# Kernel tuning notes

Hardware: AMD Instinct MI355X
Metric: run time of the kernel (lower is better)

The kernel has to match this reference:

```python
import jax, jax.numpy as jnp
import numpy as np
from jax import lax

NUM_GROUP = 512
GROUP_SIZE = 32


def fps(xyz, npoint):
    """Farthest point sampling. xyz: [B, N, 3] -> centers [B, npoint, 3]."""
    B, N, _ = xyz.shape
    big = jnp.asarray(1e10, xyz.dtype)

    def body(carry, _):
        min_d, farthest = carry  # [B, N], [B]
        centroid = jnp.take_along_axis(xyz, farthest[:, None, None], axis=1)  # [B,1,3]
        d = jnp.sum((xyz - centroid) ** 2, axis=-1)  # [B, N]
        min_d = jnp.minimum(min_d, d)
        nxt = jnp.argmax(min_d, axis=-1).astype(jnp.int32)
        return (min_d, nxt), farthest

    init = (jnp.full((B, N), big, xyz.dtype), jnp.zeros((B,), jnp.int32))
    _, idxs = lax.scan(body, init, None, length=npoint)  # [npoint, B]
    idxs = idxs.T  # [B, npoint]
    return jnp.take_along_axis(xyz, idxs[..., None], axis=1)  # [B, npoint, 3]


def knn_idx(xyz, center, k):
    """xyz [B,N,3], center [B,G,3] -> idx [B,G,k] of k nearest (squared L2)."""
    # [B, G, N] squared distances
    d2 = jnp.sum((center[:, :, None, :] - xyz[:, None, :, :]) ** 2, axis=-1)
    _, idx = lax.top_k(-d2, k)  # smallest distances
    return idx


def setup_inputs() -> dict:
    key = jax.random.key(0)
    xyz = jax.random.normal(key, (32, 3, 8192), dtype=jnp.float32)
    return {"xyz": xyz}


def reference(xyz):
    # xyz: [B, 3, N] -> [B, N, 3]
    pts = jnp.transpose(xyz, (0, 2, 1))[:, :, :3]
    B, N, _ = pts.shape
    center = fps(pts, NUM_GROUP)                  # [B, G, 3]
    idx = knn_idx(pts, center, GROUP_SIZE)        # [B, G, k]
    flat_idx = idx.reshape(B, NUM_GROUP * GROUP_SIZE)
    neighborhood = jnp.take_along_axis(pts, flat_idx[..., None], axis=1)
    neighborhood = neighborhood.reshape(B, NUM_GROUP, GROUP_SIZE, 3)
    neighborhood = neighborhood - center[:, :, None, :]
    return neighborhood, center
```

## Files before the change

kernel.cpp:

```cpp
#include <hip/hip_runtime.h>

typedef unsigned long long u64;
typedef unsigned int u32;
typedef float v2f __attribute__((ext_vector_type(2)));

#define BATCH 32
#define NPTS  8192
#define NGRP  512
#define KNN_K 32

#define FPS_T 256
#define FPS_W (FPS_T / 64)
#define PPAIR (NPTS / FPS_T / 2)
#define KNN_WPB 4
#define QCAP 128

__device__ __forceinline__ float sq3(float dx, float dy, float dz) {
    return __fadd_rn(__fadd_rn(__fmul_rn(dx, dx), __fmul_rn(dy, dy)), __fmul_rn(dz, dz));
}

__device__ __forceinline__ u64 packdi(float d, int n) {
    return ((u64)__float_as_uint(d) << 32) | (u32)n;
}

__device__ __forceinline__ u64 umin64(u64 a, u64 b) { return a < b ? a : b; }
__device__ __forceinline__ u64 umax64(u64 a, u64 b) { return a > b ? a : b; }

__device__ __forceinline__ u64 shfl_xor_u64(u64 v, int m) {
    int lo = __shfl_xor((int)(u32)v, m, 64);
    int hi = __shfl_xor((int)(u32)(v >> 32), m, 64);
    return ((u64)(u32)hi << 32) | (u32)lo;
}

__device__ __forceinline__ u64 shfl_u64(u64 v, int src) {
    int lo = __shfl((int)(u32)v, src, 64);
    int hi = __shfl((int)(u32)(v >> 32), src, 64);
    return ((u64)(u32)hi << 32) | (u32)lo;
}

template <int CTRL>
__device__ __forceinline__ u64 dpp_max_step(u64 k) {
    u32 plo = (u32)__builtin_amdgcn_update_dpp(0, (int)(u32)k, CTRL, 0xF, 0xF, true);
    u32 phi = (u32)__builtin_amdgcn_update_dpp(0, (int)(u32)(k >> 32), CTRL, 0xF, 0xF, true);
    u64 p = ((u64)phi << 32) | plo;
    return k > p ? k : p;
}
__device__ __forceinline__ u64 dpp_wave_max(u64 k) {
    k = dpp_max_step<0x111>(k);
    k = dpp_max_step<0x112>(k);
    k = dpp_max_step<0x114>(k);
    k = dpp_max_step<0x118>(k);
    k = dpp_max_step<0x142>(k);
    k = dpp_max_step<0x143>(k);
    return k;
}

__device__ __forceinline__ u64 lane_sort64(u64 v, int lane) {
#pragma unroll
    for (int k = 2; k <= 64; k <<= 1) {
#pragma unroll
        for (int j = k >> 1; j > 0; j >>= 1) {
            u64 p = shfl_xor_u64(v, j);
            bool keepmin = (((lane & k) == 0) == ((lane & j) == 0));
            u64 mn = umin64(v, p), mx = umax64(v, p);
            v = keepmin ? mn : mx;
        }
    }
    return v;
}

__device__ __forceinline__ u64 lane_merge64(u64 m, u64 c, int lane) {
    u64 cr = shfl_xor_u64(c, 63);
    u64 z = umin64(m, cr);
#pragma unroll
    for (int dd = 32; dd > 0; dd >>= 1) {
        u64 p = shfl_xor_u64(z, dd);
        u64 mn = umin64(z, p), mx = umax64(z, p);
        z = (lane & dd) ? mx : mn;
    }
    return z;
}

__global__ __launch_bounds__(FPS_T) void fps_kernel(const float* __restrict__ in,
                                                    float* __restrict__ centers) {
#pragma clang fp contract(off)
    __shared__ float sx[NPTS];
    __shared__ float sy[NPTS];
    __shared__ float sz[NPTS];
    __shared__ u64 s_key[2][FPS_W];
    __shared__ float s_out[NGRP * 3];

    const int b = blockIdx.x;
    const int t = threadIdx.x;
    const int w = t >> 6;
    const float* xp = in + (size_t)b * 3 * NPTS;
    const float* yp = xp + NPTS;
    const float* zp = xp + 2 * NPTS;

    v2f xr[PPAIR], yr[PPAIR], zr[PPAIR], md[PPAIR];
#pragma unroll
    for (int i = 0; i < PPAIR; ++i) {
        int n = i * (2 * FPS_T) + 2 * t;
        xr[i] = *(const v2f*)(xp + n);
        yr[i] = *(const v2f*)(yp + n);
        zr[i] = *(const v2f*)(zp + n);
        *(v2f*)(sx + n) = xr[i];
        *(v2f*)(sy + n) = yr[i];
        *(v2f*)(sz + n) = zr[i];
        md[i] = (v2f){1e10f, 1e10f};
    }
    __syncthreads();

    int cur = 0;
    for (int r = 0; r < NGRP; ++r) {
        const float cx = sx[cur], cy = sy[cur], cz = sz[cur];
        if (t == 0) {
            s_out[r * 3 + 0] = cx;
            s_out[r * 3 + 1] = cy;
            s_out[r * 3 + 2] = cz;
        }

        float bd0 = -1.0f, bd1 = -1.0f;
        int   bi0 = 0,     bi1 = 0;
#pragma unroll
        for (int i = 0; i < PPAIR; ++i) {
            v2f dx = xr[i] - cx;
            v2f dy = yr[i] - cy;
            v2f dz = zr[i] - cz;
            v2f dd = dx * dx + dy * dy + dz * dz;
            md[i] = __builtin_elementwise_min(md[i], dd);
            int n = i * (2 * FPS_T) + 2 * t;
            if (md[i].x > bd0) { bd0 = md[i].x; bi0 = n; }
            if (md[i].y > bd1) { bd1 = md[i].y; bi1 = n + 1; }
        }
        u64 k0 = ((u64)__float_as_uint(bd0) << 32) | (u32)(~(u32)bi0);
        u64 k1 = ((u64)__float_as_uint(bd1) << 32) | (u32)(~(u32)bi1);
        u64 k = dpp_wave_max(umax64(k0, k1));
        if ((t & 63) == 63) s_key[r & 1][w] = k;
        __syncthreads();
        u64 m = umax64(umax64(s_key[r & 1][0], s_key[r & 1][1]),
                       umax64(s_key[r & 1][2], s_key[r & 1][3]));
        cur = (int)(~(u32)m);
    }

    __syncthreads();
    float* cdst = centers + (size_t)b * NGRP * 3;
    for (int i = t; i < NGRP * 3; i += FPS_T) cdst[i] = s_out[i];
}

__global__ __launch_bounds__(KNN_WPB * 64) void knn_kernel(const float* __restrict__ in,
                                                           const float* __restrict__ centers,
                                                           float* __restrict__ out) {
    __shared__ u64 sbuf[KNN_WPB][QCAP];

    const int wave = threadIdx.x >> 6;
    const int lane = threadIdx.x & 63;
    const int cid  = blockIdx.x * KNN_WPB + wave;
    const int b    = cid >> 9;

    const float* xp = in + (size_t)b * 3 * NPTS;
    const float* yp = xp + NPTS;
    const float* zp = xp + 2 * NPTS;

    const float cx = centers[cid * 3 + 0];
    const float cy = centers[cid * 3 + 1];
    const float cz = centers[cid * 3 + 2];

    float x = xp[lane], y = yp[lane], z = zp[lane];
    u64 m = packdi(sq3(__fsub_rn(x, cx), __fsub_rn(y, cy), __fsub_rn(z, cz)), lane);
    m = lane_sort64(m, lane);
    u64 tau = shfl_u64(m, 31);
    int cnt = 0;

    float nx = xp[64 + lane], ny = yp[64 + lane], nz = zp[64 + lane];
#pragma unroll 1
    for (int j = 1; j < NPTS / 64; ++j) {
        x = nx; y = ny; z = nz;
        if (j + 1 < NPTS / 64) {
            int n2 = (j + 1) * 64 + lane;
            nx = xp[n2]; ny = yp[n2]; nz = zp[n2];
        }
        float d = sq3(__fsub_rn(x, cx), __fsub_rn(y, cy), __fsub_rn(z, cz));
        u64 kk = packdi(d, j * 64 + lane);
        bool cand = kk < tau;
        u64 mask = __ballot(cand);
        if (mask) {
            u32 below = __builtin_amdgcn_mbcnt_hi(
                (u32)(mask >> 32), __builtin_amdgcn_mbcnt_lo((u32)mask, 0));
            if (cand) sbuf[wave][cnt + below] = kk;
            cnt += (int)__popcll(mask);
            if (cnt >= 64) {
                u64 c = sbuf[wave][lane];
                c = lane_sort64(c, lane);
                m = lane_merge64(m, c, lane);
                tau = shfl_u64(m, 31);
                int rem = cnt - 64;
                if (lane < rem) sbuf[wave][lane] = sbuf[wave][64 + lane];
                cnt = rem;
            }
        }
    }
    while (cnt > 0) {
        int take = cnt < 64 ? cnt : 64;
        u64 v = sbuf[wave][lane];
        u64 c = (lane < take) ? v : ~0ull;
        c = lane_sort64(c, lane);
        m = lane_merge64(m, c, lane);
        int rem = cnt - take;
        if (lane < rem) sbuf[wave][lane] = sbuf[wave][64 + lane];
        cnt = rem;
    }

    if (lane < KNN_K) {
        int n = (int)(u32)m;
        size_t o = (size_t)cid * (KNN_K * 3) + (size_t)lane * 3;
        out[o + 0] = __fsub_rn(xp[n], cx);
        out[o + 1] = __fsub_rn(yp[n], cy);
        out[o + 2] = __fsub_rn(zp[n], cz);
    }
}

extern "C" void kernel_launch(void* const* d_in, const int* in_sizes, int n_in,
                              void* d_out, int out_size, void* d_ws, size_t ws_size,
                              hipStream_t stream) {
    const float* in  = (const float*)d_in[0];
    float* out       = (float*)d_out;
    float* centers   = out + (size_t)BATCH * NGRP * KNN_K * 3;

    fps_kernel<<<BATCH, FPS_T, 0, stream>>>(in, centers);
    knn_kernel<<<(BATCH * NGRP) / KNN_WPB, KNN_WPB * 64, 0, stream>>>(in, centers, out);
}
```

Measured before the change: 586.2 us.

## Fuse FPS and KNN into one cooperative kernel with progress-flag overlap

Merges the FPS and KNN kernels into a single cooperative launch. 32 blocks run FPS and publish centers in chunks of 16 along with a per-batch progress counter, while 224 persistent KNN blocks spin-wait on that counter and process centers as soon as they appear. This lets KNN work overlap the serial FPS loop instead of waiting for it to finish. The KNN loop is also unrolled by 4 so loads can be issued ahead. The cost is a memset, a spin-wait protocol that relies on co-residency, and fewer KNN waves than before.

```diff
diff --git a/kernel.cpp b/kernel.cpp
--- a/kernel.cpp
+++ b/kernel.cpp
@@ -14,6 +14,13 @@
 #define PPAIR (NPTS / FPS_T / 2)
 #define KNN_WPB 4
 #define QCAP 128
+
+#define FPS_BLOCKS 32
+#define KNN_BLOCKS 224
+#define TOT_BLOCKS (FPS_BLOCKS + KNN_BLOCKS)
+#define CHUNK 16
+#define TASKS (BATCH * NGRP)
+#define KNN_WAVES (KNN_BLOCKS * KNN_WPB)
 
 __device__ __forceinline__ float sq3(float dx, float dy, float dz) {
     return __fadd_rn(__fadd_rn(__fmul_rn(dx, dx), __fmul_rn(dy, dy)), __fmul_rn(dz, dz));
@@ -81,152 +88,208 @@
     return z;
 }
 
-__global__ __launch_bounds__(FPS_T) void fps_kernel(const float* __restrict__ in,
-                                                    float* __restrict__ centers) {
+__device__ __forceinline__ void knn_step(u64& m, u64& tau, int& cnt, u64* sbuf,
+                                         float x, float y, float z,
+                                         float cx, float cy, float cz,
+                                         int n, int lane) {
+    float d = sq3(__fsub_rn(x, cx), __fsub_rn(y, cy), __fsub_rn(z, cz));
+    u64 kk = packdi(d, n);
+    bool cand = kk < tau;
+    u64 mask = __ballot(cand);
+    if (mask) {
+        u32 below = __builtin_amdgcn_mbcnt_hi(
+            (u32)(mask >> 32), __builtin_amdgcn_mbcnt_lo((u32)mask, 0));
+        if (cand) sbuf[cnt + below] = kk;
+        cnt += (int)__popcll(mask);
+        if (cnt >= 64) {
+            u64 c = sbuf[lane];
+            c = lane_sort64(c, lane);
+            m = lane_merge64(m, c, lane);
+            tau = shfl_u64(m, 31);
+            int rem = cnt - 64;
+            if (lane < rem) sbuf[lane] = sbuf[64 + lane];
+            cnt = rem;
+        }
+    }
+}
+
+struct FpsS {
+    float sx[NPTS], sy[NPTS], sz[NPTS];
+    u64 s_key[2][FPS_W];
+    float s_out[NGRP * 3];
+};
+struct KnnS { u64 sbuf[KNN_WPB][QCAP]; };
+union SmemU { FpsS f; KnnS k; };
+
+__global__ __launch_bounds__(FPS_T) void fused_kernel(const float* __restrict__ in,
+                                                      float* __restrict__ gcent,
+                                                      float* __restrict__ out,
+                                                      u32* __restrict__ prog) {
+    __shared__ SmemU smem;
+    const int t = threadIdx.x;
+    const int lane = t & 63;
+
+    if (blockIdx.x < FPS_BLOCKS) {
 #pragma clang fp contract(off)
-    __shared__ float sx[NPTS];
-    __shared__ float sy[NPTS];
-    __shared__ float sz[NPTS];
-    __shared__ u64 s_key[2][FPS_W];
-    __shared__ float s_out[NGRP * 3];
-
-    const int b = blockIdx.x;
-    const int t = threadIdx.x;
-    const int w = t >> 6;
-    const float* xp = in + (size_t)b * 3 * NPTS;
-    const float* yp = xp + NPTS;
-    const float* zp = xp + 2 * NPTS;
-
-    v2f xr[PPAIR], yr[PPAIR], zr[PPAIR], md[PPAIR];
-#pragma unroll
-    for (int i = 0; i < PPAIR; ++i) {
-        int n = i * (2 * FPS_T) + 2 * t;
-        xr[i] = *(const v2f*)(xp + n);
-        yr[i] = *(const v2f*)(yp + n);
-        zr[i] = *(const v2f*)(zp + n);
-        *(v2f*)(sx + n) = xr[i];
-        *(v2f*)(sy + n) = yr[i];
-        *(v2f*)(sz + n) = zr[i];
-        md[i] = (v2f){1e10f, 1e10f};
-    }
-    __syncthreads();
-
-    int cur = 0;
-    for (int r = 0; r < NGRP; ++r) {
-        const float cx = sx[cur], cy = sy[cur], cz = sz[cur];
-        if (t == 0) {
-            s_out[r * 3 + 0] = cx;
-            s_out[r * 3 + 1] = cy;
-            s_out[r * 3 + 2] = cz;
-        }
-
-        float bd0 = -1.0f, bd1 = -1.0f;
-        int   bi0 = 0,     bi1 = 0;
+        float* sx = smem.f.sx;
+        float* sy = smem.f.sy;
+        float* sz = smem.f.sz;
+        float* s_out = smem.f.s_out;
+        const int b = blockIdx.x;
+        const int w = t >> 6;
+        const float* xp = in + (size_t)b * 3 * NPTS;
+        const float* yp = xp + NPTS;
+        const float* zp = xp + 2 * NPTS;
+        float* cdst = gcent + (size_t)b * NGRP * 3;
+
+        v2f xr[PPAIR], yr[PPAIR], zr[PPAIR], md[PPAIR];
 #pragma unroll
         for (int i = 0; i < PPAIR; ++i) {
-            v2f dx = xr[i] - cx;
-            v2f dy = yr[i] - cy;
-            v2f dz = zr[i] - cz;
-            v2f dd = dx * dx + dy * dy + dz * dz;
-            md[i] = __builtin_elementwise_min(md[i], dd);
             int n = i * (2 * FPS_T) + 2 * t;
-            if (md[i].x > bd0) { bd0 = md[i].x; bi0 = n; }
-            if (md[i].y > bd1) { bd1 = md[i].y; bi1 = n + 1; }
-        }
-        u64 k0 = ((u64)__float_as_uint(bd0) << 32) | (u32)(~(u32)bi0);
-        u64 k1 = ((u64)__float_as_uint(bd1) << 32) | (u32)(~(u32)bi1);
-        u64 k = dpp_wave_max(umax64(k0, k1));
-        if ((t & 63) == 63) s_key[r & 1][w] = k;
+            xr[i] = *(const v2f*)(xp + n);
+            yr[i] = *(const v2f*)(yp + n);
+            zr[i] = *(const v2f*)(zp + n);
+            *(v2f*)(sx + n) = xr[i];
+            *(v2f*)(sy + n) = yr[i];
+            *(v2f*)(sz + n) = zr[i];
+            md[i] = (v2f){1e10f, 1e10f};
+        }
         __syncthreads();
-        u64 m = umax64(umax64(s_key[r & 1][0], s_key[r & 1][1]),
-                       umax64(s_key[r & 1][2], s_key[r & 1][3]));
-        cur = (int)(~(u32)m);
-    }
-
-    __syncthreads();
-    float* cdst = centers + (size_t)b * NGRP * 3;
-    for (int i = t; i < NGRP * 3; i += FPS_T) cdst[i] = s_out[i];
-}
-
-__global__ __launch_bounds__(KNN_WPB * 64) void knn_kernel(const float* __restrict__ in,
-                                                           const float* __restrict__ centers,
-                                                           float* __restrict__ out) {
-    __shared__ u64 sbuf[KNN_WPB][QCAP];
-
-    const int wave = threadIdx.x >> 6;
-    const int lane = threadIdx.x & 63;
-    const int cid  = blockIdx.x * KNN_WPB + wave;
-    const int b    = cid >> 9;
-
-    const float* xp = in + (size_t)b * 3 * NPTS;
-    const float* yp = xp + NPTS;
-    const float* zp = xp + 2 * NPTS;
-
-    const float cx = centers[cid * 3 + 0];
-    const float cy = centers[cid * 3 + 1];
-    const float cz = centers[cid * 3 + 2];
-
-    float x = xp[lane], y = yp[lane], z = zp[lane];
-    u64 m = packdi(sq3(__fsub_rn(x, cx), __fsub_rn(y, cy), __fsub_rn(z, cz)), lane);
-    m = lane_sort64(m, lane);
-    u64 tau = shfl_u64(m, 31);
-    int cnt = 0;
-
-    float nx = xp[64 + lane], ny = yp[64 + lane], nz = zp[64 + lane];
+
+        int cur = 0;
+        for (int r = 0; r < NGRP; ++r) {
+            const float cx = sx[cur], cy = sy[cur], cz = sz[cur];
+            if (t == 0) {
+                s_out[r * 3 + 0] = cx;
+                s_out[r * 3 + 1] = cy;
+                s_out[r * 3 + 2] = cz;
+            }
+            float bd0 = -1.0f, bd1 = -1.0f;
+            int   bi0 = 0,     bi1 = 0;
+#pragma unroll
+            for (int i = 0; i < PPAIR; ++i) {
+                v2f dx = xr[i] - cx;
+                v2f dy = yr[i] - cy;
+                v2f dz = zr[i] - cz;
+                v2f dd = dx * dx + dy * dy + dz * dz;
+                md[i] = __builtin_elementwise_min(md[i], dd);
+                int n = i * (2 * FPS_T) + 2 * t;
+                if (md[i].x > bd0) { bd0 = md[i].x; bi0 = n; }
+                if (md[i].y > bd1) { bd1 = md[i].y; bi1 = n + 1; }
+            }
+            u64 k0 = ((u64)__float_as_uint(bd0) << 32) | (u32)(~(u32)bi0);
+            u64 k1 = ((u64)__float_as_uint(bd1) << 32) | (u32)(~(u32)bi1);
+            u64 k = dpp_wave_max(umax64(k0, k1));
+            if (lane == 63) smem.f.s_key[r & 1][w] = k;
+            __syncthreads();
+            u64 m = umax64(umax64(smem.f.s_key[r & 1][0], smem.f.s_key[r & 1][1]),
+                           umax64(smem.f.s_key[r & 1][2], smem.f.s_key[r & 1][3]));
+            cur = (int)(~(u32)m);
+
+            if ((r & (CHUNK - 1)) == (CHUNK - 1) && t < 64) {
+                int g = r >> 4;
+                if (t < CHUNK * 3) {
+                    float v = s_out[g * (CHUNK * 3) + t];
+                    __hip_atomic_store((u32*)&cdst[g * (CHUNK * 3) + t],
+                                       __float_as_uint(v), __ATOMIC_RELAXED,
+                                       __HIP_MEMORY_SCOPE_AGENT);
+                }
+                if (t == 0)
+                    __hip_atomic_store(&prog[b], (u32)(r + 1), __ATOMIC_RELEASE,
+                                       __HIP_MEMORY_SCOPE_AGENT);
+            }
+        }
+    } else {
+        const int blk = blockIdx.x - FPS_BLOCKS;
+        const int wave = t >> 6;
+        const int wid = blk * KNN_WPB + wave;
+        u64* sbuf = smem.k.sbuf[wave];
+
+        for (int tau_t = wid; tau_t < TASKS; tau_t += KNN_WAVES) {
+            const int r = tau_t >> 5;
+            const int b = tau_t & 31;
+            const int cid = (b << 9) + r;
+            const float* xp = in + (size_t)b * 3 * NPTS;
+            const float* yp = xp + NPTS;
+            const float* zp = xp + 2 * NPTS;
+
+            int pv = 0;
+            if (lane == 0)
+                pv = (int)__hip_atomic_load(&prog[b], __ATOMIC_RELAXED,
+                                            __HIP_MEMORY_SCOPE_AGENT);
+            pv = __shfl(pv, 0, 64);
+            while (pv <= r) {
+                __builtin_amdgcn_s_sleep(16);
+                if (lane == 0)
+                    pv = (int)__hip_atomic_load(&prog[b], __ATOMIC_RELAXED,
+                                                __HIP_MEMORY_SCOPE_AGENT);
+                pv = __shfl(pv, 0, 64);
+            }
+            asm volatile("" ::: "memory");
+            float ctmp = 0.f;
+            if (lane < 3)
+                ctmp = __uint_as_float(__hip_atomic_load(
+                    (const u32*)&gcent[(size_t)cid * 3 + lane], __ATOMIC_RELAXED,
+                    __HIP_MEMORY_SCOPE_AGENT));
+            const float cx = __shfl(ctmp, 0, 64);
+            const float cy = __shfl(ctmp, 1, 64);
+            const float cz = __shfl(ctmp, 2, 64);
+
+            float x = xp[lane], y = yp[lane], z = zp[lane];
+            u64 m = packdi(sq3(__fsub_rn(x, cx), __fsub_rn(y, cy), __fsub_rn(z, cz)), lane);
+            m = lane_sort64(m, lane);
+            u64 tau = shfl_u64(m, 31);
+            int cnt = 0;
+
+            int j = 1;
 #pragma unroll 1
-    for (int j = 1; j < NPTS / 64; ++j) {
-        x = nx; y = ny; z = nz;
-        if (j + 1 < NPTS / 64) {
-            int n2 = (j + 1) * 64 + lane;
-            nx = xp[n2]; ny = yp[n2]; nz = zp[n2];
-        }
-        float d = sq3(__fsub_rn(x, cx), __fsub_rn(y, cy), __fsub_rn(z, cz));
-        u64 kk = packdi(d, j * 64 + lane);
-        bool cand = kk < tau;
-        u64 mask = __ballot(cand);
-        if (mask) {
-            u32 below = __builtin_amdgcn_mbcnt_hi(
-                (u32)(mask >> 32), __builtin_amdgcn_mbcnt_lo((u32)mask, 0));
-            if (cand) sbuf[wave][cnt + below] = kk;
-            cnt += (int)__popcll(mask);
-            if (cnt >= 64) {
-                u64 c = sbuf[wave][lane];
+            for (; j + 3 < NPTS / 64; j += 4) {
+                int n0 = j * 64 + lane, n1 = n0 + 64, n2 = n0 + 128, n3 = n0 + 192;
+                float x0 = xp[n0], y0 = yp[n0], z0 = zp[n0];
+                float x1 = xp[n1], y1 = yp[n1], z1 = zp[n1];
+                float x2 = xp[n2], y2 = yp[n2], z2 = zp[n2];
+                float x3 = xp[n3], y3 = yp[n3], z3 = zp[n3];
+                knn_step(m, tau, cnt, sbuf, x0, y0, z0, cx, cy, cz, n0, lane);
+                knn_step(m, tau, cnt, sbuf, x1, y1, z1, cx, cy, cz, n1, lane);
+                knn_step(m, tau, cnt, sbuf, x2, y2, z2, cx, cy, cz, n2, lane);
+                knn_step(m, tau, cnt, sbuf, x3, y3, z3, cx, cy, cz, n3, lane);
+            }
+            for (; j < NPTS / 64; ++j) {
+                int n = j * 64 + lane;
+                knn_step(m, tau, cnt, sbuf, xp[n], yp[n], zp[n], cx, cy, cz, n, lane);
+            }
+            while (cnt > 0) {
+                int take = cnt < 64 ? cnt : 64;
+                u64 v = sbuf[lane];
+                u64 c = (lane < take) ? v : ~0ull;
                 c = lane_sort64(c, lane);
                 m = lane_merge64(m, c, lane);
-                tau = shfl_u64(m, 31);
-                int rem = cnt - 64;
-                if (lane < rem) sbuf[wave][lane] = sbuf[wave][64 + lane];
+                int rem = cnt - take;
+                if (lane < rem) sbuf[lane] = sbuf[64 + lane];
                 cnt = rem;
             }
-        }
-    }
-    while (cnt > 0) {
-        int take = cnt < 64 ? cnt : 64;
-        u64 v = sbuf[wave][lane];
-        u64 c = (lane < take) ? v : ~0ull;
-        c = lane_sort64(c, lane);
-        m = lane_merge64(m, c, lane);
-        int rem = cnt - take;
-        if (lane < rem) sbuf[wave][lane] = sbuf[wave][64 + lane];
-        cnt = rem;
-    }
-
-    if (lane < KNN_K) {
-        int n = (int)(u32)m;
-        size_t o = (size_t)cid * (KNN_K * 3) + (size_t)lane * 3;
-        out[o + 0] = __fsub_rn(xp[n], cx);
-        out[o + 1] = __fsub_rn(yp[n], cy);
-        out[o + 2] = __fsub_rn(zp[n], cz);
+            if (lane < KNN_K) {
+                int n = (int)(u32)m;
+                size_t o = (size_t)cid * (KNN_K * 3) + (size_t)lane * 3;
+                out[o + 0] = __fsub_rn(xp[n], cx);
+                out[o + 1] = __fsub_rn(yp[n], cy);
+                out[o + 2] = __fsub_rn(zp[n], cz);
+            }
+        }
     }
 }
 
 extern "C" void kernel_launch(void* const* d_in, const int* in_sizes, int n_in,
                               void* d_out, int out_size, void* d_ws, size_t ws_size,
                               hipStream_t stream) {
-    const float* in  = (const float*)d_in[0];
-    float* out       = (float*)d_out;
-    float* centers   = out + (size_t)BATCH * NGRP * KNN_K * 3;
-
-    fps_kernel<<<BATCH, FPS_T, 0, stream>>>(in, centers);
-    knn_kernel<<<(BATCH * NGRP) / KNN_WPB, KNN_WPB * 64, 0, stream>>>(in, centers, out);
-}
+    const float* in = (const float*)d_in[0];
+    float* out      = (float*)d_out;
+    float* gcent    = out + (size_t)BATCH * NGRP * KNN_K * 3;
+    u32* prog       = (u32*)d_ws;
+
+    hipMemsetAsync(prog, 0, BATCH * sizeof(u32), stream);
+
+    void* args[] = {(void*)&in, (void*)&gcent, (void*)&out, (void*)&prog};
+    hipLaunchCooperativeKernel((const void*)fused_kernel, dim3(TOT_BLOCKS),
+                               dim3(FPS_T), args, 0, stream);
+}
```

Result: no change. 592.2 us (+1.0%).

## Process two batches per FPS block with 512 threads and register-held centroids

Applied to the files above, without the earlier changes.

The FPS kernel now handles two point clouds per block using 512 threads, launching half as many blocks. The shared-memory copies of the point coordinates are removed. After each round, the thread that owns the winning point writes its coordinates from registers to shared memory, which adds a second barrier per round. Interleaving two independent reductions is meant to hide barrier and reduction latency across the 512 serial rounds. In exchange, only 16 CUs are used instead of 32, and each thread does twice the work per round.

```diff
diff --git a/kernel.cpp b/kernel.cpp
--- a/kernel.cpp
+++ b/kernel.cpp
@@ -9,7 +9,7 @@
 #define NGRP  512
 #define KNN_K 32
 
-#define FPS_T 256
+#define FPS_T 512
 #define FPS_W (FPS_T / 64)
 #define PPAIR (NPTS / FPS_T / 2)
 #define KNN_WPB 4
@@ -84,68 +84,129 @@
 __global__ __launch_bounds__(FPS_T) void fps_kernel(const float* __restrict__ in,
                                                     float* __restrict__ centers) {
 #pragma clang fp contract(off)
-    __shared__ float sx[NPTS];
-    __shared__ float sy[NPTS];
-    __shared__ float sz[NPTS];
-    __shared__ u64 s_key[2][FPS_W];
-    __shared__ float s_out[NGRP * 3];
-
-    const int b = blockIdx.x;
+    __shared__ float s_cA[3], s_cB[3];
+    __shared__ u64 s_keyA[2][FPS_W];
+    __shared__ u64 s_keyB[2][FPS_W];
+    __shared__ float s_outA[NGRP * 3];
+    __shared__ float s_outB[NGRP * 3];
+
+    const int bA = 2 * blockIdx.x;
+    const int bB = bA + 1;
     const int t = threadIdx.x;
     const int w = t >> 6;
-    const float* xp = in + (size_t)b * 3 * NPTS;
-    const float* yp = xp + NPTS;
-    const float* zp = xp + 2 * NPTS;
-
-    v2f xr[PPAIR], yr[PPAIR], zr[PPAIR], md[PPAIR];
+    const float* xpA = in + (size_t)bA * 3 * NPTS;
+    const float* ypA = xpA + NPTS;
+    const float* zpA = xpA + 2 * NPTS;
+    const float* xpB = in + (size_t)bB * 3 * NPTS;
+    const float* ypB = xpB + NPTS;
+    const float* zpB = xpB + 2 * NPTS;
+
+    v2f xrA[PPAIR], yrA[PPAIR], zrA[PPAIR], mdA[PPAIR];
+    v2f xrB[PPAIR], yrB[PPAIR], zrB[PPAIR], mdB[PPAIR];
 #pragma unroll
     for (int i = 0; i < PPAIR; ++i) {
         int n = i * (2 * FPS_T) + 2 * t;
-        xr[i] = *(const v2f*)(xp + n);
-        yr[i] = *(const v2f*)(yp + n);
-        zr[i] = *(const v2f*)(zp + n);
-        *(v2f*)(sx + n) = xr[i];
-        *(v2f*)(sy + n) = yr[i];
-        *(v2f*)(sz + n) = zr[i];
-        md[i] = (v2f){1e10f, 1e10f};
+        xrA[i] = *(const v2f*)(xpA + n);
+        yrA[i] = *(const v2f*)(ypA + n);
+        zrA[i] = *(const v2f*)(zpA + n);
+        xrB[i] = *(const v2f*)(xpB + n);
+        yrB[i] = *(const v2f*)(ypB + n);
+        zrB[i] = *(const v2f*)(zpB + n);
+        mdA[i] = (v2f){1e10f, 1e10f};
+        mdB[i] = (v2f){1e10f, 1e10f};
+    }
+    if (t == 0) {
+        s_cA[0] = xrA[0].x; s_cA[1] = yrA[0].x; s_cA[2] = zrA[0].x;
+        s_cB[0] = xrB[0].x; s_cB[1] = yrB[0].x; s_cB[2] = zrB[0].x;
     }
     __syncthreads();
 
-    int cur = 0;
     for (int r = 0; r < NGRP; ++r) {
-        const float cx = sx[cur], cy = sy[cur], cz = sz[cur];
+        const float cAx = s_cA[0], cAy = s_cA[1], cAz = s_cA[2];
+        const float cBx = s_cB[0], cBy = s_cB[1], cBz = s_cB[2];
         if (t == 0) {
-            s_out[r * 3 + 0] = cx;
-            s_out[r * 3 + 1] = cy;
-            s_out[r * 3 + 2] = cz;
+            s_outA[r * 3 + 0] = cAx; s_outA[r * 3 + 1] = cAy; s_outA[r * 3 + 2] = cAz;
+            s_outB[r * 3 + 0] = cBx; s_outB[r * 3 + 1] = cBy; s_outB[r * 3 + 2] = cBz;
         }
 
         float bd0 = -1.0f, bd1 = -1.0f;
         int   bi0 = 0,     bi1 = 0;
 #pragma unroll
         for (int i = 0; i < PPAIR; ++i) {
-            v2f dx = xr[i] - cx;
-            v2f dy = yr[i] - cy;
-            v2f dz = zr[i] - cz;
+            v2f dx = xrA[i] - cAx;
+            v2f dy = yrA[i] - cAy;
+            v2f dz = zrA[i] - cAz;
             v2f dd = dx * dx + dy * dy + dz * dz;
-            md[i] = __builtin_elementwise_min(md[i], dd);
+            mdA[i] = __builtin_elementwise_min(mdA[i], dd);
             int n = i * (2 * FPS_T) + 2 * t;
-            if (md[i].x > bd0) { bd0 = md[i].x; bi0 = n; }
-            if (md[i].y > bd1) { bd1 = md[i].y; bi1 = n + 1; }
-        }
-        u64 k0 = ((u64)__float_as_uint(bd0) << 32) | (u32)(~(u32)bi0);
-        u64 k1 = ((u64)__float_as_uint(bd1) << 32) | (u32)(~(u32)bi1);
-        u64 k = dpp_wave_max(umax64(k0, k1));
-        if ((t & 63) == 63) s_key[r & 1][w] = k;
+            if (mdA[i].x > bd0) { bd0 = mdA[i].x; bi0 = n; }
+            if (mdA[i].y > bd1) { bd1 = mdA[i].y; bi1 = n + 1; }
+        }
+        u64 kA = dpp_wave_max(umax64(
+            ((u64)__float_as_uint(bd0) << 32) | (u32)(~(u32)bi0),
+            ((u64)__float_as_uint(bd1) << 32) | (u32)(~(u32)bi1)));
+        if ((t & 63) == 63) s_keyA[r & 1][w] = kA;
+
+        bd0 = -1.0f; bd1 = -1.0f; bi0 = 0; bi1 = 0;
+#pragma unroll
+        for (int i = 0; i < PPAIR; ++i) {
+            v2f dx = xrB[i] - cBx;
+            v2f dy = yrB[i] - cBy;
+            v2f dz = zrB[i] - cBz;
+            v2f dd = dx * dx + dy * dy + dz * dz;
+            mdB[i] = __builtin_elementwise_min(mdB[i], dd);
+            int n = i * (2 * FPS_T) + 2 * t;
+            if (mdB[i].x > bd0) { bd0 = mdB[i].x; bi0 = n; }
+            if (mdB[i].y > bd1) { bd1 = mdB[i].y; bi1 = n + 1; }
+        }
+        u64 kB = dpp_wave_max(umax64(
+            ((u64)__float_as_uint(bd0) << 32) | (u32)(~(u32)bi0),
+            ((u64)__float_as_uint(bd1) << 32) | (u32)(~(u32)bi1)));
+        if ((t & 63) == 63) s_keyB[r & 1][w] = kB;
+
         __syncthreads();
-        u64 m = umax64(umax64(s_key[r & 1][0], s_key[r & 1][1]),
-                       umax64(s_key[r & 1][2], s_key[r & 1][3]));
-        cur = (int)(~(u32)m);
-    }
-
-    __syncthreads();
-    float* cdst = centers + (size_t)b * NGRP * 3;
-    for (int i = t; i < NGRP * 3; i += FPS_T) cdst[i] = s_out[i];
+
+        u64 mA = s_keyA[r & 1][0];
+        u64 mB = s_keyB[r & 1][0];
+#pragma unroll
+        for (int i = 1; i < FPS_W; ++i) {
+            mA = umax64(mA, s_keyA[r & 1][i]);
+            mB = umax64(mB, s_keyB[r & 1][i]);
+        }
+        const int curA = (int)(~(u32)mA);
+        const int curB = (int)(~(u32)mB);
+
+        if (t == ((curA >> 1) & (FPS_T - 1))) {
+            const int sl = curA >> 10, h = curA & 1;
+#pragma unroll
+            for (int i = 0; i < PPAIR; ++i) {
+                if (i == sl) {
+                    s_cA[0] = h ? xrA[i].y : xrA[i].x;
+                    s_cA[1] = h ? yrA[i].y : yrA[i].x;
+                    s_cA[2] = h ? zrA[i].y : zrA[i].x;
+                }
+            }
+        }
+        if (t == ((curB >> 1) & (FPS_T - 1))) {
+            const int sl = curB >> 10, h = curB & 1;
+#pragma unroll
+            for (int i = 0; i < PPAIR; ++i) {
+                if (i == sl) {
+                    s_cB[0] = h ? xrB[i].y : xrB[i].x;
+                    s_cB[1] = h ? yrB[i].y : yrB[i].x;
+                    s_cB[2] = h ? zrB[i].y : zrB[i].x;
+                }
+            }
+        }
+        __syncthreads();
+    }
+
+    float* cdstA = centers + (size_t)bA * NGRP * 3;
+    float* cdstB = centers + (size_t)bB * NGRP * 3;
+    for (int i = t; i < NGRP * 3; i += FPS_T) {
+        cdstA[i] = s_outA[i];
+        cdstB[i] = s_outB[i];
+    }
 }
 
 __global__ __launch_bounds__(KNN_WPB * 64) void knn_kernel(const float* __restrict__ in,
@@ -227,6 +288,6 @@
     float* out       = (float*)d_out;
     float* centers   = out + (size_t)BATCH * NGRP * KNN_K * 3;
 
-    fps_kernel<<<BATCH, FPS_T, 0, stream>>>(in, centers);
+    fps_kernel<<<BATCH / 2, FPS_T, 0, stream>>>(in, centers);
     knn_kernel<<<(BATCH * NGRP) / KNN_WPB, KNN_WPB * 64, 0, stream>>>(in, centers, out);
 }
```

After: 1.185 ms. 102% more time.

## Replace FPS block barriers with per-round LDS flag spinning and pack two batches per block

Applied to the files above, without the earlier changes.

The FPS kernel drops __syncthreads from its 512-round loop. Each round, every wave writes its argmax key into a per-round LDS slot and then spins on volatile reads until all four slots are non-zero. The owning thread publishes the next centroid into a per-round flagged float4 slot, so the xyz copies in shared memory go away. Two batches now share one 512-thread block, halving the grid, which trades the per-round barrier cost for busy-wait polling and relies on LDS visibility without explicit fences.

```diff
diff --git a/kernel.cpp b/kernel.cpp
--- a/kernel.cpp
+++ b/kernel.cpp
@@ -3,15 +3,17 @@
 typedef unsigned long long u64;
 typedef unsigned int u32;
 typedef float v2f __attribute__((ext_vector_type(2)));
+typedef float v4f __attribute__((ext_vector_type(4)));
 
 #define BATCH 32
 #define NPTS  8192
 #define NGRP  512
 #define KNN_K 32
 
-#define FPS_T 256
-#define FPS_W (FPS_T / 64)
-#define PPAIR (NPTS / FPS_T / 2)
+#define FPS_T 512
+#define SUB_T 256
+#define SUB_W 4
+#define PPAIR (NPTS / SUB_T / 2)
 #define KNN_WPB 4
 #define QCAP 128
 
@@ -84,41 +86,42 @@
 __global__ __launch_bounds__(FPS_T) void fps_kernel(const float* __restrict__ in,
                                                     float* __restrict__ centers) {
 #pragma clang fp contract(off)
-    __shared__ float sx[NPTS];
-    __shared__ float sy[NPTS];
-    __shared__ float sz[NPTS];
-    __shared__ u64 s_key[2][FPS_W];
-    __shared__ float s_out[NGRP * 3];
-
-    const int b = blockIdx.x;
+    __shared__ u64 s_key[2][NGRP][SUB_W];
+    __shared__ v4f s_c4[2][NGRP + 1];
+
     const int t = threadIdx.x;
     const int w = t >> 6;
+    const int g = w >> 2;
+    const int wg = w & 3;
+    const int tt = t & (SUB_T - 1);
+    const int lane = t & 63;
+    const int b = 2 * blockIdx.x + g;
+
     const float* xp = in + (size_t)b * 3 * NPTS;
     const float* yp = xp + NPTS;
     const float* zp = xp + 2 * NPTS;
 
+    for (int i = t; i < 2 * NGRP * SUB_W; i += FPS_T) ((u64*)s_key)[i] = 0;
+    for (int i = t; i < 2 * (NGRP + 1) * 4; i += FPS_T) ((float*)s_c4)[i] = 0.0f;
+
     v2f xr[PPAIR], yr[PPAIR], zr[PPAIR], md[PPAIR];
 #pragma unroll
     for (int i = 0; i < PPAIR; ++i) {
-        int n = i * (2 * FPS_T) + 2 * t;
+        int n = i * (2 * SUB_T) + 2 * tt;
         xr[i] = *(const v2f*)(xp + n);
         yr[i] = *(const v2f*)(yp + n);
         zr[i] = *(const v2f*)(zp + n);
-        *(v2f*)(sx + n) = xr[i];
-        *(v2f*)(sy + n) = yr[i];
-        *(v2f*)(sz + n) = zr[i];
         md[i] = (v2f){1e10f, 1e10f};
     }
     __syncthreads();
 
-    int cur = 0;
+    if (tt == 0)
+        s_c4[g][0] = (v4f){xr[0].x, yr[0].x, zr[0].x, 1.0f};
+
     for (int r = 0; r < NGRP; ++r) {
-        const float cx = sx[cur], cy = sy[cur], cz = sz[cur];
-        if (t == 0) {
-            s_out[r * 3 + 0] = cx;
-            s_out[r * 3 + 1] = cy;
-            s_out[r * 3 + 2] = cz;
-        }
+        volatile float* cw = (volatile float*)&s_c4[g][r];
+        while (cw[3] == 0.0f) { }
+        const float cx = cw[0], cy = cw[1], cz = cw[2];
 
         float bd0 = -1.0f, bd1 = -1.0f;
         int   bi0 = 0,     bi1 = 0;
@@ -129,23 +132,43 @@
             v2f dz = zr[i] - cz;
             v2f dd = dx * dx + dy * dy + dz * dz;
             md[i] = __builtin_elementwise_min(md[i], dd);
-            int n = i * (2 * FPS_T) + 2 * t;
+            int n = i * (2 * SUB_T) + 2 * tt;
             if (md[i].x > bd0) { bd0 = md[i].x; bi0 = n; }
             if (md[i].y > bd1) { bd1 = md[i].y; bi1 = n + 1; }
         }
-        u64 k0 = ((u64)__float_as_uint(bd0) << 32) | (u32)(~(u32)bi0);
-        u64 k1 = ((u64)__float_as_uint(bd1) << 32) | (u32)(~(u32)bi1);
-        u64 k = dpp_wave_max(umax64(k0, k1));
-        if ((t & 63) == 63) s_key[r & 1][w] = k;
-        __syncthreads();
-        u64 m = umax64(umax64(s_key[r & 1][0], s_key[r & 1][1]),
-                       umax64(s_key[r & 1][2], s_key[r & 1][3]));
-        cur = (int)(~(u32)m);
-    }
-
-    __syncthreads();
+        u64 k = dpp_wave_max(umax64(
+            ((u64)__float_as_uint(bd0) << 32) | (u32)(~(u32)bi0),
+            ((u64)__float_as_uint(bd1) << 32) | (u32)(~(u32)bi1)));
+        if (lane == 63) s_key[g][r][wg] = k;
+
+        volatile u64* P = (volatile u64*)&s_key[g][r][0];
+        u64 p0, p1, p2, p3;
+        do {
+            p0 = P[0]; p1 = P[1]; p2 = P[2]; p3 = P[3];
+        } while ((p0 == 0) | (p1 == 0) | (p2 == 0) | (p3 == 0));
+        u64 m = umax64(umax64(p0, p1), umax64(p2, p3));
+        const int cur = (int)(~(u32)m);
+
+        if (tt == ((cur >> 1) & (SUB_T - 1))) {
+            const int sl = cur >> 9, h = cur & 1;
+#pragma unroll
+            for (int i = 0; i < PPAIR; ++i) {
+                if (i == sl) {
+                    s_c4[g][r + 1] = (v4f){h ? xr[i].y : xr[i].x,
+                                           h ? yr[i].y : yr[i].x,
+                                           h ? zr[i].y : zr[i].x, 1.0f};
+                }
+            }
+        }
+    }
+
     float* cdst = centers + (size_t)b * NGRP * 3;
-    for (int i = t; i < NGRP * 3; i += FPS_T) cdst[i] = s_out[i];
+    for (int i = tt; i < NGRP; i += SUB_T) {
+        v4f c = s_c4[g][i];
+        cdst[i * 3 + 0] = c.x;
+        cdst[i * 3 + 1] = c.y;
+        cdst[i * 3 + 2] = c.z;
+    }
 }
 
 __global__ __launch_bounds__(KNN_WPB * 64) void knn_kernel(const float* __restrict__ in,
@@ -227,6 +250,6 @@
     float* out       = (float*)d_out;
     float* centers   = out + (size_t)BATCH * NGRP * KNN_K * 3;
 
-    fps_kernel<<<BATCH, FPS_T, 0, stream>>>(in, centers);
+    fps_kernel<<<BATCH / 2, FPS_T, 0, stream>>>(in, centers);
     knn_kernel<<<(BATCH * NGRP) / KNN_WPB, KNN_WPB * 64, 0, stream>>>(in, centers, out);
 }
```

Measured after the change: 1.030 ms. 1.76x slower.
